# Performance work log

Measured on AMD Instinct MI355X. Metric: run time of the kernel, lower is better.

Reference implementation:

```python
import math
import jax, jax.numpy as jnp
import numpy as np

B, T, C, H = 4, 2048, 1024, 16
HD = C // H

def gelu_tanh(x):
    return 0.5 * x * (1.0 + jnp.tanh(jnp.sqrt(2.0 / jnp.pi) * (x + 0.044715 * x * x * x)))

def layernorm(x, w, b, eps=1e-5):
    mu = jnp.mean(x, axis=-1, keepdims=True)
    var = jnp.var(x, axis=-1, keepdims=True)
    return (x - mu) * jax.lax.rsqrt(var + eps) * w + b

def setup_inputs() -> dict:
    key = jax.random.key(0)
    ks = jax.random.split(key, 8)
    s = 0.02
    return {
        "x": jax.random.normal(ks[0], (B, T, C), dtype=jnp.float32),
        "ln1_w": jnp.ones((C,), jnp.float32), "ln1_b": jnp.zeros((C,), jnp.float32),
        "attn_w": jax.random.normal(ks[1], (C, 3 * C), jnp.float32) * s,
        "attn_b": jnp.zeros((3 * C,), jnp.float32),
        "proj_w": jax.random.normal(ks[2], (C, C), jnp.float32) * s,
        "proj_b": jnp.zeros((C,), jnp.float32),
        "ln2_w": jnp.ones((C,), jnp.float32), "ln2_b": jnp.zeros((C,), jnp.float32),
        "fc_w": jax.random.normal(ks[3], (C, 4 * C), jnp.float32) * s,
        "fc_b": jnp.zeros((4 * C,), jnp.float32),
        "fc_proj_w": jax.random.normal(ks[4], (4 * C, C), jnp.float32) * s,
        "fc_proj_b": jnp.zeros((C,), jnp.float32),
    }

def block(x, ln1_w, ln1_b, attn_w, attn_b, proj_w, proj_b,
          ln2_w, ln2_b, fc_w, fc_b, fc_proj_w, fc_proj_b):
    # --- causal self-attention ---
    h = layernorm(x, ln1_w, ln1_b)
    qkv = h @ attn_w + attn_b                      # [B,T,3C]
    q, k, v = jnp.split(qkv, 3, axis=-1)
    q = q.reshape(B, T, H, HD).transpose(0, 2, 1, 3)  # [B,H,T,hd]
    k = k.reshape(B, T, H, HD).transpose(0, 2, 1, 3)
    v = v.reshape(B, T, H, HD).transpose(0, 2, 1, 3)
    att = jnp.einsum('bhqd,bhkd->bhqk', q, k) * (1.0 / math.sqrt(HD))
    mask = jnp.tril(jnp.ones((T, T), dtype=bool))
    att = jnp.where(mask, att, -jnp.inf)
    att = jax.nn.softmax(att, axis=-1)
    y = jnp.einsum('bhqk,bhkd->bhqd', att, v)
    y = y.transpose(0, 2, 1, 3).reshape(B, T, C)
    x = x + (y @ proj_w + proj_b)
    # --- MLP ---
    h = layernorm(x, ln2_w, ln2_b)
    h = gelu_tanh(h @ fc_w + fc_b)
    x = x + (h @ fc_proj_w + fc_proj_b)
    return x

def reference(x, ln1_w, ln1_b, attn_w, attn_b, proj_w, proj_b,
              ln2_w, ln2_b, fc_w, fc_b, fc_proj_w, fc_proj_b):
    return block(x, ln1_w, ln1_b, attn_w, attn_b, proj_w, proj_b,
                 ln2_w, ln2_b, fc_w, fc_b, fc_proj_w, fc_proj_b)
```

## Files before the change

### kernel.cpp

```cpp
#include <hip/hip_runtime.h>
#include <stdint.h>

#define TSEQ 2048
#define CDIM 1024
#define NHEAD 16
#define HDIM 64
#define NROWS 8192

typedef __bf16 bf16x8 __attribute__((ext_vector_type(8)));
typedef float f32x4 __attribute__((ext_vector_type(4)));
typedef float f32x16 __attribute__((ext_vector_type(16)));

__device__ __forceinline__ unsigned short f2bf(float f) {
  unsigned u = __builtin_bit_cast(unsigned, f);
  u = u + 0x7fffu + ((u >> 16) & 1u);
  return (unsigned short)(u >> 16);
}

__device__ __forceinline__ unsigned cvt_pk_bf16(float a, float b) {
  unsigned r;
  asm("v_cvt_pk_bf16_f32 %0, %1, %2" : "=v"(r) : "v"(a), "v"(b));
  return r;
}

__device__ __forceinline__ float gelu_f(float x) {
  float x3 = x * x * x;
  float z = 0.7978845608028654f * (x + 0.044715f * x3);
  float e = __expf(2.f * z);
  float t = 1.f - 2.f / (e + 1.f);
  return 0.5f * x * (1.f + t);
}

__device__ __forceinline__ void ldg_lds16(void* lds, const void* gsrc) {
  __builtin_amdgcn_global_load_lds(
      (__attribute__((address_space(1))) unsigned int*)(uintptr_t)gsrc,
      (__attribute__((address_space(3))) unsigned int*)lds,
      16, 0, 0);
}

__global__ __launch_bounds__(256) void k_wtrans(const float* __restrict__ W,
                                                unsigned short* __restrict__ Wt,
                                                int K, int N) {
  __shared__ unsigned short tl[32][40];
  int n0 = blockIdx.x * 32, k0 = blockIdx.y * 32;
  int tid = threadIdx.x;
  int r = tid >> 3, c4 = (tid & 7) * 4;
  float4 v = *(const float4*)(W + (size_t)(k0 + r) * N + n0 + c4);
  ushort4 o;
  o.x = f2bf(v.x); o.y = f2bf(v.y); o.z = f2bf(v.z); o.w = f2bf(v.w);
  *(ushort4*)&tl[r][c4] = o;
  __syncthreads();
  int n = tid >> 3, k4 = (tid & 7) * 4;
  ushort4 w;
  w.x = tl[k4 + 0][n]; w.y = tl[k4 + 1][n]; w.z = tl[k4 + 2][n]; w.w = tl[k4 + 3][n];
  *(ushort4*)(Wt + (size_t)(n0 + n) * K + k0 + k4) = w;
}

__global__ __launch_bounds__(256) void k_ln(const float* __restrict__ x,
                                            const float* __restrict__ w,
                                            const float* __restrict__ b,
                                            unsigned short* __restrict__ out) {
  int row = blockIdx.x;
  int tid = threadIdx.x;
  const float* xr = x + (size_t)row * CDIM;
  float4 v = *(const float4*)(xr + tid * 4);
  float s = v.x + v.y + v.z + v.w;
  float s2 = v.x * v.x + v.y * v.y + v.z * v.z + v.w * v.w;
#pragma unroll
  for (int off = 32; off; off >>= 1) {
    s += __shfl_xor(s, off);
    s2 += __shfl_xor(s2, off);
  }
  __shared__ float rbuf[8];
  int wv = tid >> 6, lane = tid & 63;
  if (lane == 0) { rbuf[wv] = s; rbuf[4 + wv] = s2; }
  __syncthreads();
  float S1 = rbuf[0] + rbuf[1] + rbuf[2] + rbuf[3];
  float S2 = rbuf[4] + rbuf[5] + rbuf[6] + rbuf[7];
  float mean = S1 * (1.f / CDIM);
  float var = S2 * (1.f / CDIM) - mean * mean;
  float rstd = rsqrtf(var + 1e-5f);
  float4 wv4 = *(const float4*)(w + tid * 4);
  float4 bv4 = *(const float4*)(b + tid * 4);
  ushort4 o;
  o.x = f2bf((v.x - mean) * rstd * wv4.x + bv4.x);
  o.y = f2bf((v.y - mean) * rstd * wv4.y + bv4.y);
  o.z = f2bf((v.z - mean) * rstd * wv4.z + bv4.z);
  o.w = f2bf((v.w - mean) * rstd * wv4.w + bv4.w);
  *(ushort4*)(out + (size_t)row * CDIM + tid * 4) = o;
}

template <int EPI>
__global__ __launch_bounds__(512, 4)
void k_gemm(const unsigned short* __restrict__ A,
            const unsigned short* __restrict__ Bt,
            const float* __restrict__ bias,
            const float* __restrict__ resid,
            void* __restrict__ Cout,
            int M, int N, int K) {
  constexpr int ABYTES = 128 * 64;
  constexpr int BBYTES = 256 * 64;
  constexpr int BUFSZ = ABYTES + BBYTES;
  __shared__ __align__(16) char lds[3 * BUFSZ];
  const int tid = threadIdx.x;
  const int wid = tid >> 6, lane = tid & 63;
  const int wm = wid >> 2, wn = wid & 3;
  const int fr = lane & 15, fq = lane >> 4;

  const int gx = gridDim.x;
  int flat = blockIdx.y * gx + blockIdx.x;
  {
    const int nwg = gx * gridDim.y;
    int q = nwg >> 3, r = nwg & 7;
    int xcd = flat & 7, idx = flat >> 3;
    flat = (xcd < r ? xcd * (q + 1) : r * (q + 1) + (xcd - r) * q) + idx;
  }
  const int bx = flat % gx, by = flat / gx;
  const long brow = (long)by * 128, bcol = (long)bx * 256;

  const int sby = (((lane & 3) ^ ((lane >> 3) & 3)) << 4);
  const char* gA = (const char*)(A + (size_t)(brow + wid * 16 + (lane >> 2)) * K) + sby;
  const char* gB = (const char*)(Bt + (size_t)(bcol + wid * 32 + (lane >> 2)) * K) + sby;

  const int NT = K >> 5;

#define STAGE_A(tt, bf)                                                 \
  ldg_lds16(lds + (bf) * BUFSZ + wid * 1024, gA + (size_t)(tt) * 64)
#define STAGE_B(tt, bf)                                                 \
  do {                                                                  \
    char* d_ = lds + (bf) * BUFSZ + ABYTES + wid * 2048;                \
    ldg_lds16(d_, gB + (size_t)(tt) * 64);                              \
    ldg_lds16(d_ + 1024, gB + (size_t)16 * K * 2 + (size_t)(tt) * 64);  \
  } while (0)

  STAGE_A(0, 0); STAGE_B(0, 0);
  STAGE_A(1, 1); STAGE_B(1, 1);

  f32x4 acc[4][4];
  const f32x4 vzero = {0.f, 0.f, 0.f, 0.f};
#pragma unroll
  for (int m = 0; m < 4; ++m)
#pragma unroll
    for (int n = 0; n < 4; ++n) acc[m][n] = vzero;

  const int ksw = ((fq ^ ((fr >> 1) & 3)) << 4);
  int buf = 0;
  for (int t = 0; t < NT; ++t) {
    if (t + 1 < NT) asm volatile("s_waitcnt vmcnt(3)" ::: "memory");
    else            asm volatile("s_waitcnt vmcnt(0)" ::: "memory");
    __builtin_amdgcn_s_barrier();
    __builtin_amdgcn_sched_barrier(0);
    const char* pA = lds + buf * BUFSZ;
    const char* pB = pA + ABYTES;
    int nbuf = buf + 2; if (nbuf >= 3) nbuf -= 3;
    if (t + 2 < NT) { STAGE_A(t + 2, nbuf); STAGE_B(t + 2, nbuf); }
    bf16x8 af[4], bfr[4];
#pragma unroll
    for (int m = 0; m < 4; ++m)
      af[m] = *(const bf16x8*)(pA + (wm * 64 + m * 16 + fr) * 64 + ksw);
#pragma unroll
    for (int n = 0; n < 4; ++n)
      bfr[n] = *(const bf16x8*)(pB + (wn * 64 + n * 16 + fr) * 64 + ksw);
    __builtin_amdgcn_s_setprio(1);
#pragma unroll
    for (int m = 0; m < 4; ++m)
#pragma unroll
      for (int n = 0; n < 4; ++n)
        acc[m][n] = __builtin_amdgcn_mfma_f32_16x16x32_bf16(af[m], bfr[n], acc[m][n], 0, 0, 0);
    __builtin_amdgcn_s_setprio(0);
    __builtin_amdgcn_sched_barrier(0);
    buf = buf + 1; if (buf == 3) buf = 0;
  }
#undef STAGE_A
#undef STAGE_B

#pragma unroll
  for (int m = 0; m < 4; ++m) {
    long row = brow + wm * 64 + m * 16 + fq * 4;
#pragma unroll
    for (int n = 0; n < 4; ++n) {
      long col = bcol + wn * 64 + n * 16 + fr;
      float bv = bias[col];
#pragma unroll
      for (int r = 0; r < 4; ++r) {
        float v = acc[m][n][r] + bv;
        long idx = (row + r) * (long)N + col;
        if (EPI == 0) {
          ((unsigned short*)Cout)[idx] = f2bf(v);
        } else if (EPI == 1) {
          ((unsigned short*)Cout)[idx] = f2bf(gelu_f(v));
        } else {
          ((float*)Cout)[idx] = v + resid[idx];
        }
      }
    }
  }
}

__global__ __launch_bounds__(256) void k_build_vt(const unsigned short* __restrict__ qkv,
                                                  unsigned short* __restrict__ vt) {
  __shared__ __align__(16) unsigned short tl[64][80];
  int bh = blockIdx.x, b = bh >> 4, h = bh & 15;
  int t0 = blockIdx.y * 64;
  int tid = threadIdx.x;
  int r = tid >> 2, cb = (tid & 3) * 16;
  const unsigned short* src =
      qkv + (size_t)(b * TSEQ + t0 + r) * (3 * CDIM) + 2 * CDIM + h * HDIM + cb;
  *(uint4*)&tl[r][cb] = *(const uint4*)src;
  *(uint4*)&tl[r][cb + 8] = *(const uint4*)(src + 8);
  __syncthreads();
  int d = tid >> 2, tb = (tid & 3) * 16;
  union { unsigned short u[16]; uint4 v[2]; } o;
#pragma unroll
  for (int j = 0; j < 16; ++j) o.u[j] = tl[tb + j][d];
  unsigned short* dst = vt + ((size_t)bh * HDIM + d) * TSEQ + t0 + tb;
  *(uint4*)dst = o.v[0];
  *(uint4*)(dst + 8) = o.v[1];
}

struct QSt {
  f32x16 OTlo, OThi;
  float m, l;
};

__device__ __forceinline__ void attn_qk_sm_pv(
    const bf16x8& k0, const bf16x8& k1, const bf16x8& k2, const bf16x8& k3,
    const bf16x8& v0, const bf16x8& v1, const bf16x8& v2, const bf16x8& v3,
    const bf16x8& q0f, const bf16x8& q1f, const bf16x8& q2f, const bf16x8& q3f,
    QSt& S, bool diag, int lq, int hi) {
  const float SC = 0.125f * 1.44269504088896f;
  f32x16 st;
#pragma unroll
  for (int r = 0; r < 16; ++r) st[r] = 0.f;
  __builtin_amdgcn_s_setprio(1);
  st = __builtin_amdgcn_mfma_f32_32x32x16_bf16(k0, q0f, st, 0, 0, 0);
  st = __builtin_amdgcn_mfma_f32_32x32x16_bf16(k1, q1f, st, 0, 0, 0);
  st = __builtin_amdgcn_mfma_f32_32x32x16_bf16(k2, q2f, st, 0, 0, 0);
  st = __builtin_amdgcn_mfma_f32_32x32x16_bf16(k3, q3f, st, 0, 0, 0);
  __builtin_amdgcn_s_setprio(0);
#pragma unroll
  for (int r = 0; r < 16; ++r) st[r] *= SC;
  if (diag) {
#pragma unroll
    for (int r = 0; r < 16; ++r) {
      int kvl = (r & 3) + 8 * (r >> 2) + 4 * hi;
      if (kvl > lq) st[r] = -1e30f;
    }
  }
  float tmax = st[0];
#pragma unroll
  for (int r = 1; r < 16; ++r) tmax = fmaxf(tmax, st[r]);
  float tm = fmaxf(tmax, __shfl_xor(tmax, 32));
  if (__any(tm > S.m + 8.f)) {
    float mnew = fmaxf(S.m, tm);
    float alpha = __builtin_amdgcn_exp2f(S.m - mnew);
    S.m = mnew;
    S.OTlo *= alpha;
    S.OThi *= alpha;
    S.l *= alpha;
  }
  unsigned c[8];
  float rs = 0.f;
#pragma unroll
  for (int i = 0; i < 8; ++i) {
    float pa = __builtin_amdgcn_exp2f(st[2 * i] - S.m);
    float pb = __builtin_amdgcn_exp2f(st[2 * i + 1] - S.m);
    rs += pa + pb;
    c[i] = cvt_pk_bf16(pa, pb);
  }
  S.l += rs + __shfl_xor(rs, 32);
  unsigned pc[8];
#pragma unroll
  for (int i = 0; i < 8; ++i) pc[i] = __shfl_xor(c[i], 32);
  uint4 w1, w2;
  w1.x = hi ? pc[2] : c[0]; w1.y = hi ? pc[3] : c[1];
  w1.z = hi ? c[2] : pc[0]; w1.w = hi ? c[3] : pc[1];
  w2.x = hi ? pc[6] : c[4]; w2.y = hi ? pc[7] : c[5];
  w2.z = hi ? c[6] : pc[4]; w2.w = hi ? c[7] : pc[5];
  bf16x8 f1 = __builtin_bit_cast(bf16x8, w1);
  bf16x8 f2 = __builtin_bit_cast(bf16x8, w2);
  __builtin_amdgcn_s_setprio(1);
  S.OTlo = __builtin_amdgcn_mfma_f32_32x32x16_bf16(v0, f1, S.OTlo, 0, 0, 0);
  S.OTlo = __builtin_amdgcn_mfma_f32_32x32x16_bf16(v1, f2, S.OTlo, 0, 0, 0);
  S.OThi = __builtin_amdgcn_mfma_f32_32x32x16_bf16(v2, f1, S.OThi, 0, 0, 0);
  S.OThi = __builtin_amdgcn_mfma_f32_32x32x16_bf16(v3, f2, S.OThi, 0, 0, 0);
  __builtin_amdgcn_s_setprio(0);
}

__global__ __launch_bounds__(256, 2) void k_attn(const unsigned short* __restrict__ qkv,
                                                 const unsigned short* __restrict__ vt,
                                                 unsigned short* __restrict__ y) {
  __shared__ __align__(16) unsigned short Ks[2][2][2048];
  __shared__ __align__(16) unsigned short Vs[2][2][2048];
  const int bh = blockIdx.x, b = bh >> 4, h = bh & 15;
  const int wv = threadIdx.x >> 6, lane = threadIdx.x & 63;
  const int by = blockIdx.y;
  const int w = by * 4 + wv;
  const int lq = lane & 31, hi = lane >> 5;
  const int ntL = w, ntH = 63 - w;
  const int q0L = w * 32, q0H = (63 - w) * 32;
  const int T = 64 - 4 * by;

  const unsigned short* qrowL = qkv + ((size_t)(b * TSEQ) + q0L + lq) * (3 * CDIM) + h * HDIM;
  const unsigned short* qrowH = qkv + ((size_t)(b * TSEQ) + q0H + lq) * (3 * CDIM) + h * HDIM;
  bf16x8 qL0 = *(const bf16x8*)(qrowL + 0 + hi * 8);
  bf16x8 qL1 = *(const bf16x8*)(qrowL + 16 + hi * 8);
  bf16x8 qL2 = *(const bf16x8*)(qrowL + 32 + hi * 8);
  bf16x8 qL3 = *(const bf16x8*)(qrowL + 48 + hi * 8);
  bf16x8 qH0 = *(const bf16x8*)(qrowH + 0 + hi * 8);
  bf16x8 qH1 = *(const bf16x8*)(qrowH + 16 + hi * 8);
  bf16x8 qH2 = *(const bf16x8*)(qrowH + 32 + hi * 8);
  bf16x8 qH3 = *(const bf16x8*)(qrowH + 48 + hi * 8);

  const int kr = lane & 31, kc = wv * 2 + (lane >> 5);
  const unsigned short* gK =
      qkv + ((size_t)(b * TSEQ) + kr) * (3 * CDIM) + CDIM + h * HDIM + kc * 8;
  const unsigned short* gV = vt + ((size_t)bh * HDIM + lane) * TSEQ + wv * 8;

#define STAGEKV2(pb, tt)                                                       \
  do {                                                                         \
    ldg_lds16((char*)Ks[pb][0] + wv * 1024, gK + (size_t)(tt) * 32 * (3 * CDIM));     \
    ldg_lds16((char*)Vs[pb][0] + wv * 1024, gV + (size_t)(tt) * 32);           \
    ldg_lds16((char*)Ks[pb][1] + wv * 1024, gK + (size_t)(tt + 1) * 32 * (3 * CDIM)); \
    ldg_lds16((char*)Vs[pb][1] + wv * 1024, gV + (size_t)(tt + 1) * 32);       \
  } while (0)

  QSt SL, SH;
#pragma unroll
  for (int r = 0; r < 16; ++r) {
    SL.OTlo[r] = 0.f; SL.OThi[r] = 0.f; SH.OTlo[r] = 0.f; SH.OThi[r] = 0.f;
  }
  SL.m = -1e30f; SL.l = 0.f; SH.m = -1e30f; SH.l = 0.f;

  STAGEKV2(0, 0);
  for (int tt = 0; tt < T; tt += 2) {
    __syncthreads();
    const int pb = (tt >> 1) & 1;
    if (tt + 2 < T) STAGEKV2(pb ^ 1, tt + 2);
#pragma unroll
    for (int sub = 0; sub < 2; ++sub) {
      const int t = tt + sub;
      if (t <= ntH) {
        const unsigned short* Kb = Ks[pb][sub];
        const unsigned short* Vb = Vs[pb][sub];
        bf16x8 k0 = *(const bf16x8*)(Kb + (0 + hi) * 256 + lq * 8);
        bf16x8 k1 = *(const bf16x8*)(Kb + (2 + hi) * 256 + lq * 8);
        bf16x8 k2 = *(const bf16x8*)(Kb + (4 + hi) * 256 + lq * 8);
        bf16x8 k3 = *(const bf16x8*)(Kb + (6 + hi) * 256 + lq * 8);
        bf16x8 v0 = *(const bf16x8*)(Vb + hi * 512 + lq * 8);
        bf16x8 v1 = *(const bf16x8*)(Vb + (2 + hi) * 512 + lq * 8);
        bf16x8 v2 = *(const bf16x8*)(Vb + hi * 512 + (lq + 32) * 8);
        bf16x8 v3 = *(const bf16x8*)(Vb + (2 + hi) * 512 + (lq + 32) * 8);
        attn_qk_sm_pv(k0, k1, k2, k3, v0, v1, v2, v3,
                      qH0, qH1, qH2, qH3, SH, t == ntH, lq, hi);
        if (t <= ntL)
          attn_qk_sm_pv(k0, k1, k2, k3, v0, v1, v2, v3,
                        qL0, qL1, qL2, qL3, SL, t == ntL, lq, hi);
      }
    }
  }
#undef STAGEKV2

  {
    float inv = 1.f / SH.l;
    unsigned short* yrow = y + ((size_t)(b * TSEQ) + q0H + lq) * CDIM + h * HDIM;
#pragma unroll
    for (int r = 0; r < 16; r += 2) {
      int d = (r & 3) + 8 * (r >> 2) + 4 * hi;
      unsigned lo0 = f2bf(SH.OTlo[r] * inv), lo1 = f2bf(SH.OTlo[r + 1] * inv);
      *(unsigned*)(yrow + d) = lo0 | (lo1 << 16);
      unsigned h0 = f2bf(SH.OThi[r] * inv), h1 = f2bf(SH.OThi[r + 1] * inv);
      *(unsigned*)(yrow + 32 + d) = h0 | (h1 << 16);
    }
  }
  {
    float inv = 1.f / SL.l;
    unsigned short* yrow = y + ((size_t)(b * TSEQ) + q0L + lq) * CDIM + h * HDIM;
#pragma unroll
    for (int r = 0; r < 16; r += 2) {
      int d = (r & 3) + 8 * (r >> 2) + 4 * hi;
      unsigned lo0 = f2bf(SL.OTlo[r] * inv), lo1 = f2bf(SL.OTlo[r + 1] * inv);
      *(unsigned*)(yrow + d) = lo0 | (lo1 << 16);
      unsigned h0 = f2bf(SL.OThi[r] * inv), h1 = f2bf(SL.OThi[r + 1] * inv);
      *(unsigned*)(yrow + 32 + d) = h0 | (h1 << 16);
    }
  }
}

extern "C" void kernel_launch(void* const* d_in, const int* in_sizes, int n_in,
                              void* d_out, int out_size, void* d_ws, size_t ws_size,
                              hipStream_t stream) {
  const float* x = (const float*)d_in[0];
  const float* ln1_w = (const float*)d_in[1];
  const float* ln1_b = (const float*)d_in[2];
  const float* attn_w = (const float*)d_in[3];
  const float* attn_b = (const float*)d_in[4];
  const float* proj_w = (const float*)d_in[5];
  const float* proj_b = (const float*)d_in[6];
  const float* ln2_w = (const float*)d_in[7];
  const float* ln2_b = (const float*)d_in[8];
  const float* fc_w = (const float*)d_in[9];
  const float* fc_b = (const float*)d_in[10];
  const float* fc_proj_w = (const float*)d_in[11];
  const float* fc_proj_b = (const float*)d_in[12];

  char* ws = (char*)d_ws;
  unsigned short* wt_attn = (unsigned short*)(ws + 0);
  unsigned short* wt_proj = (unsigned short*)(ws + 6291456);
  unsigned short* wt_fc = (unsigned short*)(ws + 8388608);
  unsigned short* wt_fcp = (unsigned short*)(ws + 16777216);
  float* x1 = (float*)(ws + 25165824);
  unsigned short* hbuf = (unsigned short*)(ws + 58720256);
  unsigned short* ybuf = (unsigned short*)(ws + 75497472);
  unsigned short* qkvb = (unsigned short*)(ws + 92274688);
  unsigned short* vtb = (unsigned short*)(ws + 142606336);
  unsigned short* gbuf = (unsigned short*)(ws + 92274688);

  k_wtrans<<<dim3(3072 / 32, 1024 / 32), 256, 0, stream>>>(attn_w, wt_attn, 1024, 3072);
  k_wtrans<<<dim3(1024 / 32, 1024 / 32), 256, 0, stream>>>(proj_w, wt_proj, 1024, 1024);
  k_wtrans<<<dim3(4096 / 32, 1024 / 32), 256, 0, stream>>>(fc_w, wt_fc, 1024, 4096);
  k_wtrans<<<dim3(1024 / 32, 4096 / 32), 256, 0, stream>>>(fc_proj_w, wt_fcp, 4096, 1024);

  k_ln<<<NROWS, 256, 0, stream>>>(x, ln1_w, ln1_b, hbuf);

  k_gemm<0><<<dim3(3072 / 256, NROWS / 128), 512, 0, stream>>>(
      hbuf, wt_attn, attn_b, nullptr, qkvb, NROWS, 3072, 1024);

  k_build_vt<<<dim3(64, TSEQ / 64), 256, 0, stream>>>(qkvb, vtb);

  k_attn<<<dim3(64, 8), 256, 0, stream>>>(qkvb, vtb, ybuf);

  k_gemm<2><<<dim3(1024 / 256, NROWS / 128), 512, 0, stream>>>(
      ybuf, wt_proj, proj_b, x, x1, NROWS, 1024, 1024);

  k_ln<<<NROWS, 256, 0, stream>>>(x1, ln2_w, ln2_b, hbuf);

  k_gemm<1><<<dim3(4096 / 256, NROWS / 128), 512, 0, stream>>>(
      hbuf, wt_fc, fc_b, nullptr, gbuf, NROWS, 4096, 1024);

  k_gemm<2><<<dim3(1024 / 256, NROWS / 128), 512, 0, stream>>>(
      gbuf, wt_fcp, fc_proj_b, x1, (float*)d_out, NROWS, 1024, 4096);
}
```

Before: 367.0 us.

## Store intermediate residual in bf16 and stage four KV tiles per attention iteration

The post-attention residual x1 is now written as bf16 instead of fp32. It is read back as bf16 by the second layernorm and by the final GEMM epilogue, which roughly halves the traffic for that buffer. The attention kernel also stages four 32-row K/V tiles per pipeline step instead of two, which doubles its LDS usage and halves the number of barriers. The trade-offs are lower precision on the residual path and higher LDS pressure, which may reduce occupancy for the launch_bounds(256,2) attention kernel.

```diff
diff --git a/kernel.cpp b/kernel.cpp
--- a/kernel.cpp
+++ b/kernel.cpp
@@ -15,6 +15,10 @@
   unsigned u = __builtin_bit_cast(unsigned, f);
   u = u + 0x7fffu + ((u >> 16) & 1u);
   return (unsigned short)(u >> 16);
+}
+
+__device__ __forceinline__ float bf2f(unsigned short u) {
+  return __builtin_bit_cast(float, (unsigned)u << 16);
 }
 
 __device__ __forceinline__ unsigned cvt_pk_bf16(float a, float b) {
@@ -56,14 +60,20 @@
   *(ushort4*)(Wt + (size_t)(n0 + n) * K + k0 + k4) = w;
 }
 
-__global__ __launch_bounds__(256) void k_ln(const float* __restrict__ x,
+template <int IN>
+__global__ __launch_bounds__(256) void k_ln(const void* __restrict__ xin,
                                             const float* __restrict__ w,
                                             const float* __restrict__ b,
                                             unsigned short* __restrict__ out) {
   int row = blockIdx.x;
   int tid = threadIdx.x;
-  const float* xr = x + (size_t)row * CDIM;
-  float4 v = *(const float4*)(xr + tid * 4);
+  float4 v;
+  if (IN == 0) {
+    v = *(const float4*)((const float*)xin + (size_t)row * CDIM + tid * 4);
+  } else {
+    ushort4 u = *(const ushort4*)((const unsigned short*)xin + (size_t)row * CDIM + tid * 4);
+    v.x = bf2f(u.x); v.y = bf2f(u.y); v.z = bf2f(u.z); v.w = bf2f(u.w);
+  }
   float s = v.x + v.y + v.z + v.w;
   float s2 = v.x * v.x + v.y * v.y + v.z * v.z + v.w * v.w;
 #pragma unroll
@@ -95,7 +105,7 @@
 void k_gemm(const unsigned short* __restrict__ A,
             const unsigned short* __restrict__ Bt,
             const float* __restrict__ bias,
-            const float* __restrict__ resid,
+            const void* __restrict__ resid,
             void* __restrict__ Cout,
             int M, int N, int K) {
   constexpr int ABYTES = 128 * 64;
@@ -189,8 +199,10 @@
           ((unsigned short*)Cout)[idx] = f2bf(v);
         } else if (EPI == 1) {
           ((unsigned short*)Cout)[idx] = f2bf(gelu_f(v));
+        } else if (EPI == 3) {
+          ((unsigned short*)Cout)[idx] = f2bf(v + ((const float*)resid)[idx]);
         } else {
-          ((float*)Cout)[idx] = v + resid[idx];
+          ((float*)Cout)[idx] = v + bf2f(((const unsigned short*)resid)[idx]);
         }
       }
     }
@@ -290,8 +302,8 @@
 __global__ __launch_bounds__(256, 2) void k_attn(const unsigned short* __restrict__ qkv,
                                                  const unsigned short* __restrict__ vt,
                                                  unsigned short* __restrict__ y) {
-  __shared__ __align__(16) unsigned short Ks[2][2][2048];
-  __shared__ __align__(16) unsigned short Vs[2][2][2048];
+  __shared__ __align__(16) unsigned short Ks[2][4][2048];
+  __shared__ __align__(16) unsigned short Vs[2][4][2048];
   const int bh = blockIdx.x, b = bh >> 4, h = bh & 15;
   const int wv = threadIdx.x >> 6, lane = threadIdx.x & 63;
   const int by = blockIdx.y;
@@ -317,12 +329,14 @@
       qkv + ((size_t)(b * TSEQ) + kr) * (3 * CDIM) + CDIM + h * HDIM + kc * 8;
   const unsigned short* gV = vt + ((size_t)bh * HDIM + lane) * TSEQ + wv * 8;
 
-#define STAGEKV2(pb, tt)                                                       \
-  do {                                                                         \
-    ldg_lds16((char*)Ks[pb][0] + wv * 1024, gK + (size_t)(tt) * 32 * (3 * CDIM));     \
-    ldg_lds16((char*)Vs[pb][0] + wv * 1024, gV + (size_t)(tt) * 32);           \
-    ldg_lds16((char*)Ks[pb][1] + wv * 1024, gK + (size_t)(tt + 1) * 32 * (3 * CDIM)); \
-    ldg_lds16((char*)Vs[pb][1] + wv * 1024, gV + (size_t)(tt + 1) * 32);       \
+#define STAGEKV4(pb, tt)                                                        \
+  do {                                                                          \
+    _Pragma("unroll")                                                           \
+    for (int s_ = 0; s_ < 4; ++s_) {                                            \
+      ldg_lds16((char*)Ks[pb][s_] + wv * 1024,                                  \
+                gK + (size_t)(tt + s_) * 32 * (3 * CDIM));                      \
+      ldg_lds16((char*)Vs[pb][s_] + wv * 1024, gV + (size_t)(tt + s_) * 32);    \
+    }                                                                           \
   } while (0)
 
   QSt SL, SH;
@@ -332,13 +346,13 @@
   }
   SL.m = -1e30f; SL.l = 0.f; SH.m = -1e30f; SH.l = 0.f;
 
-  STAGEKV2(0, 0);
-  for (int tt = 0; tt < T; tt += 2) {
+  STAGEKV4(0, 0);
+  for (int tt = 0; tt < T; tt += 4) {
     __syncthreads();
-    const int pb = (tt >> 1) & 1;
-    if (tt + 2 < T) STAGEKV2(pb ^ 1, tt + 2);
-#pragma unroll
-    for (int sub = 0; sub < 2; ++sub) {
+    const int pb = (tt >> 2) & 1;
+    if (tt + 4 < T) STAGEKV4(pb ^ 1, tt + 4);
+#pragma unroll
+    for (int sub = 0; sub < 4; ++sub) {
       const int t = tt + sub;
       if (t <= ntH) {
         const unsigned short* Kb = Ks[pb][sub];
@@ -359,7 +373,7 @@
       }
     }
   }
-#undef STAGEKV2
+#undef STAGEKV4
 
   {
     float inv = 1.f / SH.l;
@@ -409,7 +423,7 @@
   unsigned short* wt_proj = (unsigned short*)(ws + 6291456);
   unsigned short* wt_fc = (unsigned short*)(ws + 8388608);
   unsigned short* wt_fcp = (unsigned short*)(ws + 16777216);
-  float* x1 = (float*)(ws + 25165824);
+  unsigned short* x1 = (unsigned short*)(ws + 25165824);
   unsigned short* hbuf = (unsigned short*)(ws + 58720256);
   unsigned short* ybuf = (unsigned short*)(ws + 75497472);
   unsigned short* qkvb = (unsigned short*)(ws + 92274688);
@@ -421,7 +435,7 @@
   k_wtrans<<<dim3(4096 / 32, 1024 / 32), 256, 0, stream>>>(fc_w, wt_fc, 1024, 4096);
   k_wtrans<<<dim3(1024 / 32, 4096 / 32), 256, 0, stream>>>(fc_proj_w, wt_fcp, 4096, 1024);
 
-  k_ln<<<NROWS, 256, 0, stream>>>(x, ln1_w, ln1_b, hbuf);
+  k_ln<0><<<NROWS, 256, 0, stream>>>(x, ln1_w, ln1_b, hbuf);
 
   k_gemm<0><<<dim3(3072 / 256, NROWS / 128), 512, 0, stream>>>(
       hbuf, wt_attn, attn_b, nullptr, qkvb, NROWS, 3072, 1024);
@@ -430,14 +444,14 @@
 
   k_attn<<<dim3(64, 8), 256, 0, stream>>>(qkvb, vtb, ybuf);
 
-  k_gemm<2><<<dim3(1024 / 256, NROWS / 128), 512, 0, stream>>>(
+  k_gemm<3><<<dim3(1024 / 256, NROWS / 128), 512, 0, stream>>>(
       ybuf, wt_proj, proj_b, x, x1, NROWS, 1024, 1024);
 
-  k_ln<<<NROWS, 256, 0, stream>>>(x1, ln2_w, ln2_b, hbuf);
+  k_ln<1><<<NROWS, 256, 0, stream>>>(x1, ln2_w, ln2_b, hbuf);
 
   k_gemm<1><<<dim3(4096 / 256, NROWS / 128), 512, 0, stream>>>(
       hbuf, wt_fc, fc_b, nullptr, gbuf, NROWS, 4096, 1024);
 
-  k_gemm<2><<<dim3(1024 / 256, NROWS / 128), 512, 0, stream>>>(
+  k_gemm<4><<<dim3(1024 / 256, NROWS / 128), 512, 0, stream>>>(
       gbuf, wt_fcp, fc_proj_b, x1, (float*)d_out, NROWS, 1024, 4096);
 }
```

Measured after the change: 359.2 us, median of 3. 1.02x faster.
